# Optimization experiments

Hardware: AMD Instinct MI355X
Metric: run time of the kernel (lower is better)

The kernel has to match this reference:

```python
import jax, jax.numpy as jnp
import numpy as np

EOS = 1  # EOS_VALUE in the original code (word_label == 1 triggers end_sentence)
L_LAYERS = 2
B, T, H, E = 128, 256, 1024, 1024  # TD == E == input_size


def setup_inputs() -> dict:
    key = jax.random.key(0)
    ks = jax.random.split(key, 20)
    k = 1.0 / np.sqrt(H)
    u = lambda kk, shape: jax.random.uniform(kk, shape, jnp.float32, -k, k)
    inp = {
        "yy_pad": jax.random.randint(ks[0], (B, T), 0, E, dtype=jnp.int32),
        "h_t": jax.random.normal(ks[1], (L_LAYERS, B, H), jnp.float32),
        "h_t_rev": jax.random.normal(ks[2], (L_LAYERS, B, H), jnp.float32),
        "x_lens": jax.random.randint(ks[3], (B,), 1, T - 1, dtype=jnp.int32).at[0].set(T - 1),
        # parameters (layer 0 input size == E == H, so weights stack cleanly)
        "emb": jax.random.normal(ks[4], (E, E), jnp.float32) * 0.02,
        "W_ih": u(ks[5], (L_LAYERS, 4 * H, E)),
        "W_hh": u(ks[6], (L_LAYERS, 4 * H, H)),
        "b_ih": u(ks[7], (L_LAYERS, 4 * H)),
        "b_hh": u(ks[8], (L_LAYERS, 4 * H)),
        "W_ih_rev": u(ks[9], (L_LAYERS, 4 * H, E)),
        "W_hh_rev": u(ks[10], (L_LAYERS, 4 * H, H)),
        "b_ih_rev": u(ks[11], (L_LAYERS, 4 * H)),
        "b_hh_rev": u(ks[12], (L_LAYERS, 4 * H)),
        "c0": jnp.zeros((L_LAYERS, H), jnp.float32),
        "c0_rev": jnp.zeros((L_LAYERS, H), jnp.float32),
        "fc_W": u(ks[13], (E, 2 * H)),
        "fc_b": u(ks[14], (E,)),
    }
    return inp


def _lstm_cell(x, h, c, Wih, Whh, bih, bhh):
    # torch.nn.LSTMCell gate order: input, forget, cell(g), output
    z = x @ Wih.T + bih + h @ Whh.T + bhh  # [B, 4H]
    i, f, g, o = jnp.split(z, 4, axis=-1)
    c2 = jax.nn.sigmoid(f) * c + jax.nn.sigmoid(i) * jnp.tanh(g)
    h2 = jax.nn.sigmoid(o) * jnp.tanh(c2)
    return h2, c2


def reference(yy_pad, h_t, h_t_rev, x_lens, emb, W_ih, W_hh, b_ih, b_hh,
              W_ih_rev, W_hh_rev, b_ih_rev, b_hh_rev, c0, c0_rev, fc_W, fc_b):
    batch = yy_pad.shape[0]
    n_steps = yy_pad.shape[1]  # == max(x_lens) + 1 by construction (static)
    eos_onehot = jax.nn.one_hot(EOS, fc_W.shape[0], dtype=fc_W.dtype)  # [TD]

    c_init = jnp.broadcast_to(c0[:, None, :], (L_LAYERS, batch, c0.shape[1]))
    c_init_rev = jnp.broadcast_to(c0_rev[:, None, :], (L_LAYERS, batch, c0.shape[1]))

    def step(carry, _):
        feed, h, hr, c, cr, ended = carry
        x = emb[feed]   # [B, E]  (sos embedding / previous argmax token)
        xr = x
        hs, hrs, cs, crs = [], [], [], []
        for l in range(L_LAYERS):
            hn, cn = _lstm_cell(x, h[l], c[l], W_ih[l], W_hh[l], b_ih[l], b_hh[l])
            hrn, crn = _lstm_cell(xr, hr[l], cr[l], W_ih_rev[l], W_hh_rev[l], b_ih_rev[l], b_hh_rev[l])
            hs.append(hn); cs.append(cn); hrs.append(hrn); crs.append(crn)
            x, xr = hn, hrn
        h, hr = jnp.stack(hs), jnp.stack(hrs)
        c, cr = jnp.stack(cs), jnp.stack(crs)
        # faithful to torch: cat([B,H],[B,H]) -> [B,2H] -> permute(1,0) -> reshape(B,-1)
        wh = jnp.concatenate([h[-1], hr[-1]], axis=-1).T.reshape(batch, -1)
        logits = wh @ fc_W.T + fc_b  # [B, TD]
        logits = jnp.where(ended[:, None], eos_onehot, logits)
        label = jnp.argmax(logits, axis=1).astype(jnp.int32)
        ended = ended | (label == EOS)
        return (label, h, hr, c, cr, ended), logits

    carry0 = (yy_pad[:, 0], h_t, h_t_rev, c_init, c_init_rev,
              jnp.zeros((batch,), jnp.bool_))
    _, logits_seq = jax.lax.scan(step, carry0, None, length=n_steps)  # [T, B, TD]
    return jax.nn.softmax(jnp.transpose(logits_seq, (1, 0, 2)), axis=-1)  # [B, T, TD]
```

## Files before the change

### kernel.cpp

```cpp
#include <hip/hip_runtime.h>
#include <math.h>

#define NB 128
#define NT 256
#define NH 1024
#define NE 1024
#define G4 4096
#define EOSL 1

#define C_OFF    ((size_t)0)
#define HT_OFF   ((size_t)524288)
#define FCZ_OFF  ((size_t)786432)
#define BIAS_OFF ((size_t)2883584)
#define END_OFF  ((size_t)2899968)
#define XPH_OFF  ((size_t)2900096)
#define XPX_OFF  ((size_t)3948672)
#define WP_OFF   ((size_t)4079744)
#define TOTAL_MIN_F  ((size_t)4079744)
#define TOTAL_PACK_F ((size_t)37634176)

typedef __attribute__((ext_vector_type(8))) short s8v;
typedef __attribute__((ext_vector_type(4))) float f4v;

__device__ __forceinline__ float sigmoid_stable(float x) {
  if (x >= 0.f) return 1.f / (1.f + expf(-x));
  float ex = expf(x);
  return ex / (1.f + ex);
}
__device__ __forceinline__ void add4(float4& d, const float4 a) {
  d.x += a.x; d.y += a.y; d.z += a.z; d.w += a.w;
}
__device__ __forceinline__ unsigned short bf_rne(float x) {
  unsigned u = __float_as_uint(x);
  return (unsigned short)((u + 0x7FFFu + ((u >> 16) & 1u)) >> 16);
}
__device__ __forceinline__ void split_bf(float x, unsigned short& h, unsigned short& l) {
  unsigned u = __float_as_uint(x);
  unsigned hb = (u + 0x7FFFu + ((u >> 16) & 1u)) >> 16;
  h = (unsigned short)hb;
  float r = x - __uint_as_float(hb << 16);
  l = bf_rne(r);
}
__device__ __forceinline__ void cvt8(float4 a0, float4 a1, s8v& hi, s8v& lo)
{
  const float v[8] = {a0.x, a0.y, a0.z, a0.w, a1.x, a1.y, a1.z, a1.w};
  #pragma unroll
  for (int j = 0; j < 8; j++) {
    unsigned short h, l; split_bf(v[j], h, l);
    hi[j] = (short)h; lo[j] = (short)l;
  }
}


__global__ void k_init(const int* yy, const float* h_t, const float* h_tr,
                       const float* c0, const float* c0r,
                       const float* b_ih, const float* b_hh,
                       const float* b_ihr, const float* b_hhr,
                       const float* emb,
                       unsigned short* xph, unsigned short* xpx,
                       float* call, float* bias, int* ended)
{
  int idx = blockIdx.x * 256 + threadIdx.x;
  if (idx < 2 * 2048 * 128) {
    int dir = idx / (2048 * 128); int rem = idx % (2048 * 128);
    int row = rem >> 7, b = rem & 127;
    int l = row >> 10, n = row & 1023;
    const float* src = dir ? h_tr : h_t;
    float v = src[((size_t)l * 128 + b) * 1024 + n];
    unsigned short h, lo; split_bf(v, h, lo);
    size_t off = ((size_t)(dir * 64 + (row >> 5)) * 8 + (b >> 4)) * 1024
               + ((b & 15) + 16 * ((n >> 3) & 3)) * 8 + (n & 7);
    xph[off] = h; xph[off + 512] = lo;
  }
  if (idx < 4 * 1024 * 128) {
    int ld = idx / (1024 * 128); int l = ld >> 1;
    int rem = idx % (1024 * 128);
    int n = rem >> 7;
    const float* cs = (ld & 1) ? c0r : c0;
    call[idx] = cs[l * 1024 + n];
  }
  if (idx < 4 * 4096) {
    int ld = idx / 4096; int l = ld >> 1, dir = ld & 1;
    int m = idx & 4095;
    bias[idx] = (dir ? b_ihr : b_ih)[l * 4096 + m] + (dir ? b_hhr : b_hh)[l * 4096 + m];
  }
  if (idx < 128 * 1024) {
    int b = idx >> 10, k = idx & 1023;
    int e = yy[b * NT];
    float v = emb[(size_t)e * 1024 + k];
    unsigned short h, lo; split_bf(v, h, lo);
    size_t off = ((size_t)(k >> 5) * 8 + (b >> 4)) * 1024
               + ((b & 15) + 16 * ((k >> 3) & 3)) * 8 + (k & 7);
    xpx[off] = h; xpx[off + 512] = lo;
  }
  if (idx < NB) ended[idx] = 0;
}

__global__ void k_packW(const float* W_ih, const float* W_hh,
                        const float* W_ihr, const float* W_hhr,
                        unsigned short* WP)
{
  int idx = blockIdx.x * 256 + threadIdx.x;
  int l = idx & 63;
  int frag = idx >> 6;
  int ktile = frag & 63;
  int mq = (frag >> 6) & 255;
  int ld = frag >> 14;
  int layer = ld >> 1, dir = ld & 1;
  int s = l & 15;
  int gate = s >> 2;
  int m = gate * 1024 + mq * 4 + (s & 3);
  int kg = ktile * 32 + (l >> 4) * 8;
  const float* base;
  if (kg < 1024) base = (dir ? W_ihr : W_ih) + ((size_t)layer * 4096 + m) * 1024 + kg;
  else           base = (dir ? W_hhr : W_hh) + ((size_t)layer * 4096 + m) * 1024 + (kg - 1024);
  float4 a0 = *(const float4*)base, a1 = *(const float4*)(base + 4);
  s8v hi, lo; cvt8(a0, a1, hi, lo);
  unsigned short* outp = WP + (size_t)frag * 1024 + l * 8;
  *(s8v*)outp = hi;
  *(s8v*)(outp + 512) = lo;
}

__device__ __forceinline__ void red_write8(float* red, int slot, int l, const f4v (&acc)[8])
{
  #pragma unroll
  for (int bt = 0; bt < 8; bt++)
    *(f4v*)&red[(size_t)slot * 2048 + bt * 256 + l * 4] = acc[bt];
}
__device__ __forceinline__ void red_add8(const float* red, int slot, int l, f4v (&acc)[8])
{
  #pragma unroll
  for (int bt = 0; bt < 8; bt++)
    acc[bt] += *(const f4v*)&red[(size_t)slot * 2048 + bt * 256 + l * 4];
}
__device__ __forceinline__ void gloadB(const unsigned short* Bb, int kk,
                                       s8v (&h)[8], s8v (&lo)[8])
{
  #pragma unroll
  for (int bt = 0; bt < 8; bt++) {
    const unsigned short* q = Bb + ((size_t)(kk * 8 + bt) << 10);
    h[bt] = *(const s8v*)q; lo[bt] = *(const s8v*)(q + 512);
  }
}

struct CellP {
  const unsigned short* WP;
  const float* Wih; const float* Whh; const float* Wihr; const float* Whhr;
  const float* bias; float* c; const unsigned short* xpx; float* Ht;
};

template<int LAYER, int PACKED>
__global__ __launch_bounds__(512, 4) void k_cell(CellP p, const unsigned short* xpR,
                                                 unsigned short* xpW)
{
  __shared__ __align__(16) float lds[10240];
  const int mq = blockIdx.x, dir = blockIdx.y, tid = threadIdx.x;
  const int l = tid & 63, w = tid >> 6;
  const int lr = l & 15, lk = l >> 4;

  const unsigned short* Bb;
  if (LAYER == 0)
    Bb = (w < 4) ? p.xpx + (size_t)w * 65536
                 : xpR + (size_t)(dir * 64 + (w - 4) * 8) * 8192;
  else
    Bb = (w < 4) ? xpW + (size_t)(dir * 64 + w * 8) * 8192
                 : xpR + (size_t)(dir * 64 + 32 + (w - 4) * 8) * 8192;
  Bb += l * 8;

  f4v acc[8];
  #pragma unroll
  for (int bt = 0; bt < 8; bt++) acc[bt] = (f4v)(0.0f);

  if (PACKED) {
    const unsigned short* Wb = p.WP + (size_t)(LAYER * 2 + dir) * 16777216ULL
        + (((size_t)mq * 64 + (size_t)w * 8) << 10) + l * 8;
    s8v whc = *(const s8v*)Wb, wlc = *(const s8v*)(Wb + 512);
    #pragma unroll 1
    for (int kk = 0; kk < 8; kk++) {
      s8v bh[8], bl[8];
      gloadB(Bb, kk, bh, bl);
      s8v whn, wln;
      if (kk < 7) {
        const unsigned short* q = Wb + ((size_t)(kk + 1) << 10);
        whn = *(const s8v*)q; wln = *(const s8v*)(q + 512);
      }
      #pragma unroll
      for (int bt = 0; bt < 8; bt++) {
        acc[bt] = __builtin_amdgcn_mfma_f32_16x16x32_bf16(whc, bh[bt], acc[bt], 0, 0, 0);
        acc[bt] = __builtin_amdgcn_mfma_f32_16x16x32_bf16(whc, bl[bt], acc[bt], 0, 0, 0);
        acc[bt] = __builtin_amdgcn_mfma_f32_16x16x32_bf16(wlc, bh[bt], acc[bt], 0, 0, 0);
      }
      if (kk < 7) { whc = whn; wlc = wln; }
    }
  } else {
    const float* Wsel = ((w < 4) ? (dir ? p.Wihr : p.Wih) : (dir ? p.Whhr : p.Whh))
                      + (size_t)LAYER * 4194304;
    int col0 = (w & 3) * 256 + lk * 8;
    int m = (lr >> 2) * 1024 + mq * 4 + (lr & 3);
    const float* Wr = Wsel + (size_t)m * 1024 + col0;
    float4 ac0 = *(const float4*)Wr, ac1 = *(const float4*)(Wr + 4);
    #pragma unroll 1
    for (int kk = 0; kk < 8; kk++) {
      s8v bh[8], bl[8];
      gloadB(Bb, kk, bh, bl);
      float4 an0, an1;
      if (kk < 7) {
        an0 = *(const float4*)(Wr + (kk + 1) * 32);
        an1 = *(const float4*)(Wr + (kk + 1) * 32 + 4);
      }
      s8v wh, wl;
      cvt8(ac0, ac1, wh, wl);
      #pragma unroll
      for (int bt = 0; bt < 8; bt++) {
        acc[bt] = __builtin_amdgcn_mfma_f32_16x16x32_bf16(wh, bh[bt], acc[bt], 0, 0, 0);
        acc[bt] = __builtin_amdgcn_mfma_f32_16x16x32_bf16(wh, bl[bt], acc[bt], 0, 0, 0);
        acc[bt] = __builtin_amdgcn_mfma_f32_16x16x32_bf16(wl, bh[bt], acc[bt], 0, 0, 0);
      }
      if (kk < 7) { ac0 = an0; ac1 = an1; }
    }
  }

  if (w >= 4) red_write8(lds, w - 4, l, acc);
  __syncthreads();
  if (w < 4) red_add8(lds, w, l, acc);
  __syncthreads();
  if (w == 2 || w == 3) red_write8(lds, w - 2, l, acc);
  __syncthreads();
  if (w < 2) red_add8(lds, w, l, acc);
  __syncthreads();
  if (w < 2) red_write8(lds, w, l, acc);
  __syncthreads();
  float* zs = lds + 8192;
  {
    f4v s = *(const f4v*)&lds[(size_t)tid * 4];
    s += *(const f4v*)&lds[2048 + (size_t)tid * 4];
    int bt = tid >> 6, ll = tid & 63;
    #pragma unroll
    for (int r = 0; r < 4; r++)
      zs[((ll >> 4) * 4 + r) * 128 + bt * 16 + (ll & 15)] = s[r];
  }
  __syncthreads();

  {
    int ldg = LAYER * 2 + dir;
    int b = tid & 127, nl = tid >> 7;
    int n = mq * 4 + nl;
    float iv = zs[nl * 128 + b]        + p.bias[ldg * 4096 + n];
    float fv = zs[(4 + nl) * 128 + b]  + p.bias[ldg * 4096 + 1024 + n];
    float gv = zs[(8 + nl) * 128 + b]  + p.bias[ldg * 4096 + 2048 + n];
    float ov = zs[(12 + nl) * 128 + b] + p.bias[ldg * 4096 + 3072 + n];
    float* cp = p.c + ((size_t)ldg * 1024 + n) * 128 + b;
    float cold = *cp;
    float cn = sigmoid_stable(fv) * cold + sigmoid_stable(iv) * tanhf(gv);
    float hn = sigmoid_stable(ov) * tanhf(cn);
    *cp = cn;
    unsigned short hh, lo; split_bf(hn, hh, lo);
    int kt = LAYER * 32 + (n >> 5), n5 = n & 31;
    size_t off = ((size_t)(dir * 64 + kt) * 8 + (b >> 4)) * 1024
               + ((size_t)((b & 15) + 16 * ((n5 >> 3) & 3))) * 8 + (n5 & 7);
    xpW[off] = hh;
    xpW[off + 512] = lo;
    if (LAYER == 1)
      p.Ht[(size_t)dir * 131072 + (size_t)n * 128 + b] = hn;
  }
}

__global__ __launch_bounds__(256) void k_fc(const float* Ht, const float* fc_W, float* fcz)
{
  int et = blockIdx.x, kp = blockIdx.y;
  int e0 = et * 64;
  int k00 = kp * 128;
  __shared__ __align__(16) float in_s[128][36];
  __shared__ __align__(16) float w_s[64][36];
  int t = threadIdx.x, e_sub = t & 7, bg = t >> 3, b0 = bg * 4;
  float acc[8][4] = {};
  for (int kc = 0; kc < 128; kc += 32) {
    #pragma unroll
    for (int i = 0; i < 4; i++) {
      int flat = t + 256 * i, r = flat >> 3, f4i = flat & 7;
      float4 v = *(const float4*)(Ht + (size_t)r * 2048 + k00 + kc + f4i * 4);
      int sw = (f4i ^ (r >> 2)) & 7;
      *(float4*)&in_s[r][sw * 4] = v;
    }
    #pragma unroll
    for (int i = 0; i < 2; i++) {
      int flat = t + 256 * i, r = flat >> 3, f4i = flat & 7;
      *(float4*)&w_s[r][f4i * 4] =
          *(const float4*)(fc_W + (size_t)(e0 + r) * 2048 + k00 + kc + f4i * 4);
    }
    __syncthreads();
    #pragma unroll
    for (int kq = 0; kq < 8; kq++) {
      int ksw = (kq ^ bg) & 7;
      float4 a4[4];
      #pragma unroll
      for (int ib = 0; ib < 4; ib++) a4[ib] = *(const float4*)&in_s[b0 + ib][ksw * 4];
      float4 w4[8];
      #pragma unroll
      for (int je = 0; je < 8; je++) w4[je] = *(const float4*)&w_s[e_sub + 8 * je][kq * 4];
      #pragma unroll
      for (int je = 0; je < 8; je++)
        #pragma unroll
        for (int ib = 0; ib < 4; ib++)
          acc[je][ib] += a4[ib].x * w4[je].x + a4[ib].y * w4[je].y +
                         a4[ib].z * w4[je].z + a4[ib].w * w4[je].w;
    }
    __syncthreads();
  }
  for (int je = 0; je < 8; je++) {
    int e = e0 + e_sub + 8 * je;
    for (int ib = 0; ib < 4; ib++)
      fcz[((size_t)kp * NB + b0 + ib) * NE + e] = acc[je][ib];
  }
}

__global__ void k_final(const float* fcz, const float* fc_b, int* ended,
                        float* out, int tstep, const float* emb, unsigned short* xpx)
{
  int b = blockIdx.x;
  int t = threadIdx.x;
  __shared__ float sval[256];
  __shared__ int   sidx[256];
  __shared__ float ssum[256];
  bool end = (ended[b] != 0);
  float v[4];
  int e_base = t * 4;
  float4 vv = *(const float4*)&fc_b[e_base];
  #pragma unroll
  for (int p = 0; p < 16; p++)
    add4(vv, *(const float4*)&fcz[((size_t)p * NB + b) * NE + e_base]);
  v[0] = vv.x; v[1] = vv.y; v[2] = vv.z; v[3] = vv.w;
  if (end) {
    #pragma unroll
    for (int j = 0; j < 4; j++) v[j] = (e_base + j == EOSL) ? 1.f : 0.f;
  }
  float bv = v[0]; int bi = e_base;
  #pragma unroll
  for (int j = 1; j < 4; j++) if (v[j] > bv) { bv = v[j]; bi = e_base + j; }
  sval[t] = bv; sidx[t] = bi;
  __syncthreads();
  for (int s = 128; s > 0; s >>= 1) {
    if (t < s) {
      float ov = sval[t + s]; int oi = sidx[t + s];
      if (ov > sval[t] || (ov == sval[t] && oi < sidx[t])) { sval[t] = ov; sidx[t] = oi; }
    }
    __syncthreads();
  }
  float m = sval[0]; int label = sidx[0];
  {
    int k0 = t * 4;
    float4 e4 = *(const float4*)(emb + (size_t)label * 1024 + k0);
    size_t off = ((size_t)(k0 >> 5) * 8 + (b >> 4)) * 1024
               + ((b & 15) + 16 * ((k0 >> 3) & 3)) * 8 + (k0 & 7);
    ushort4 h4, l4;
    unsigned short hh, ll;
    split_bf(e4.x, hh, ll); h4.x = hh; l4.x = ll;
    split_bf(e4.y, hh, ll); h4.y = hh; l4.y = ll;
    split_bf(e4.z, hh, ll); h4.z = hh; l4.z = ll;
    split_bf(e4.w, hh, ll); h4.w = hh; l4.w = ll;
    *(ushort4*)(xpx + off) = h4;
    *(ushort4*)(xpx + off + 512) = l4;
  }
  float ls = 0.f;
  #pragma unroll
  for (int j = 0; j < 4; j++) { v[j] = expf(v[j] - m); ls += v[j]; }
  ssum[t] = ls;
  __syncthreads();
  for (int s = 128; s > 0; s >>= 1) { if (t < s) ssum[t] += ssum[t + s]; __syncthreads(); }
  float inv = 1.f / ssum[0];
  float* orow = out + ((size_t)b * NT + tstep) * NE + e_base;
  #pragma unroll
  for (int j = 0; j < 4; j++) orow[j] = v[j] * inv;
  if (t == 0) ended[b] = (end || label == EOSL) ? 1 : 0;
}

extern "C" void kernel_launch(void* const* d_in, const int* in_sizes, int n_in,
                              void* d_out, int out_size, void* d_ws, size_t ws_size,
                              hipStream_t stream)
{
  const int*   yy    = (const int*)d_in[0];
  const float* h_t   = (const float*)d_in[1];
  const float* h_tr  = (const float*)d_in[2];
  const float* emb   = (const float*)d_in[4];
  const float* W_ih  = (const float*)d_in[5];
  const float* W_hh  = (const float*)d_in[6];
  const float* b_ih  = (const float*)d_in[7];
  const float* b_hh  = (const float*)d_in[8];
  const float* W_ihr = (const float*)d_in[9];
  const float* W_hhr = (const float*)d_in[10];
  const float* b_ihr = (const float*)d_in[11];
  const float* b_hhr = (const float*)d_in[12];
  const float* c0    = (const float*)d_in[13];
  const float* c0r   = (const float*)d_in[14];
  const float* fc_W  = (const float*)d_in[15];
  const float* fc_b  = (const float*)d_in[16];
  float* out = (float*)d_out;

  float* ws = (float*)d_ws;
  float* call = ws + C_OFF;
  float* Ht   = ws + HT_OFF;
  float* fcz  = ws + FCZ_OFF;
  float* bias = ws + BIAS_OFF;
  int* ended  = (int*)(ws + END_OFF);
  unsigned short* xph = (unsigned short*)(ws + XPH_OFF);
  unsigned short* xpx = (unsigned short*)(ws + XPX_OFF);
  unsigned short* WP  = (unsigned short*)(ws + WP_OFF);
  bool packed = ws_size >= TOTAL_PACK_F * sizeof(float);

  k_init<<<2048, 256, 0, stream>>>(yy, h_t, h_tr, c0, c0r, b_ih, b_hh, b_ihr, b_hhr,
                                   emb, xph, xpx, call, bias, ended);
  if (packed)
    k_packW<<<16384, 256, 0, stream>>>(W_ih, W_hh, W_ihr, W_hhr, WP);

  CellP cp;
  cp.WP = WP;
  cp.Wih = W_ih; cp.Whh = W_hh; cp.Wihr = W_ihr; cp.Whhr = W_hhr;
  cp.bias = bias; cp.c = call; cp.xpx = xpx; cp.Ht = Ht;

  for (int t = 0; t < NT; t++) {
    const unsigned short* xpR = xph + (size_t)(t & 1) * 1048576;
    unsigned short* xpW = xph + (size_t)((t & 1) ^ 1) * 1048576;
    if (packed) {
      k_cell<0, 1><<<dim3(256, 2), 512, 0, stream>>>(cp, xpR, xpW);
      k_cell<1, 1><<<dim3(256, 2), 512, 0, stream>>>(cp, xpR, xpW);
    } else {
      k_cell<0, 0><<<dim3(256, 2), 512, 0, stream>>>(cp, xpR, xpW);
      k_cell<1, 0><<<dim3(256, 2), 512, 0, stream>>>(cp, xpR, xpW);
    }
    k_fc<<<dim3(16, 16), 256, 0, stream>>>(Ht, fc_W, fcz);
    k_final<<<128, 256, 0, stream>>>(fcz, fc_b, ended, out, t, emb, xpx);
  }
}
```

Measured before the change: 21.25 ms.

## Replace FP32 FC GEMM with split-bf16 MFMA kernel writing pre-packed fragments

```diff
diff --git a/kernel.cpp b/kernel.cpp
--- a/kernel.cpp
+++ b/kernel.cpp
@@ -9,15 +9,16 @@
 #define EOSL 1
 
 #define C_OFF    ((size_t)0)
-#define HT_OFF   ((size_t)524288)
-#define FCZ_OFF  ((size_t)786432)
-#define BIAS_OFF ((size_t)2883584)
-#define END_OFF  ((size_t)2899968)
-#define XPH_OFF  ((size_t)2900096)
-#define XPX_OFF  ((size_t)3948672)
-#define WP_OFF   ((size_t)4079744)
-#define TOTAL_MIN_F  ((size_t)4079744)
-#define TOTAL_PACK_F ((size_t)37634176)
+#define FCL_OFF  ((size_t)524288)
+#define XFC_OFF  ((size_t)655360)
+#define BIAS_OFF ((size_t)917504)
+#define END_OFF  ((size_t)933888)
+#define XPH_OFF  ((size_t)934016)
+#define XPX_OFF  ((size_t)1982592)
+#define FCWP_OFF ((size_t)2113664)
+#define WP_OFF   ((size_t)4210816)
+#define TOTAL_MIN_F  ((size_t)4210816)
+#define TOTAL_PACK_F ((size_t)37765248)
 
 typedef __attribute__((ext_vector_type(8))) short s8v;
 typedef __attribute__((ext_vector_type(4))) float f4v;
@@ -26,9 +27,6 @@
   if (x >= 0.f) return 1.f / (1.f + expf(-x));
   float ex = expf(x);
   return ex / (1.f + ex);
-}
-__device__ __forceinline__ void add4(float4& d, const float4 a) {
-  d.x += a.x; d.y += a.y; d.z += a.z; d.w += a.w;
 }
 __device__ __forceinline__ unsigned short bf_rne(float x) {
   unsigned u = __float_as_uint(x);
@@ -98,27 +96,43 @@
 
 __global__ void k_packW(const float* W_ih, const float* W_hh,
                         const float* W_ihr, const float* W_hhr,
-                        unsigned short* WP)
+                        const float* fc_W,
+                        unsigned short* WP, unsigned short* fcWP)
 {
   int idx = blockIdx.x * 256 + threadIdx.x;
-  int l = idx & 63;
-  int frag = idx >> 6;
-  int ktile = frag & 63;
-  int mq = (frag >> 6) & 255;
-  int ld = frag >> 14;
-  int layer = ld >> 1, dir = ld & 1;
-  int s = l & 15;
-  int gate = s >> 2;
-  int m = gate * 1024 + mq * 4 + (s & 3);
-  int kg = ktile * 32 + (l >> 4) * 8;
-  const float* base;
-  if (kg < 1024) base = (dir ? W_ihr : W_ih) + ((size_t)layer * 4096 + m) * 1024 + kg;
-  else           base = (dir ? W_hhr : W_hh) + ((size_t)layer * 4096 + m) * 1024 + (kg - 1024);
-  float4 a0 = *(const float4*)base, a1 = *(const float4*)(base + 4);
-  s8v hi, lo; cvt8(a0, a1, hi, lo);
-  unsigned short* outp = WP + (size_t)frag * 1024 + l * 8;
-  *(s8v*)outp = hi;
-  *(s8v*)(outp + 512) = lo;
+  if (idx < 4194304) {
+    int l = idx & 63;
+    int frag = idx >> 6;
+    int ktile = frag & 63;
+    int mq = (frag >> 6) & 255;
+    int ld = frag >> 14;
+    int layer = ld >> 1, dir = ld & 1;
+    int s = l & 15;
+    int gate = s >> 2;
+    int m = gate * 1024 + mq * 4 + (s & 3);
+    int kg = ktile * 32 + (l >> 4) * 8;
+    const float* base;
+    if (kg < 1024) base = (dir ? W_ihr : W_ih) + ((size_t)layer * 4096 + m) * 1024 + kg;
+    else           base = (dir ? W_hhr : W_hh) + ((size_t)layer * 4096 + m) * 1024 + (kg - 1024);
+    float4 a0 = *(const float4*)base, a1 = *(const float4*)(base + 4);
+    s8v hi, lo; cvt8(a0, a1, hi, lo);
+    unsigned short* outp = WP + (size_t)frag * 1024 + l * 8;
+    *(s8v*)outp = hi;
+    *(s8v*)(outp + 512) = lo;
+  } else if (idx < 4456448) {
+    int i2 = idx - 4194304;
+    int l = i2 & 63;
+    int frag = i2 >> 6;
+    int ktile = frag & 63, mq = frag >> 6;
+    int m = mq * 16 + (l & 15);
+    int kg = ktile * 32 + (l >> 4) * 8;
+    const float* base = fc_W + (size_t)m * 2048 + kg;
+    float4 a0 = *(const float4*)base, a1 = *(const float4*)(base + 4);
+    s8v hi, lo; cvt8(a0, a1, hi, lo);
+    unsigned short* outp = fcWP + (size_t)frag * 1024 + l * 8;
+    *(s8v*)outp = hi;
+    *(s8v*)(outp + 512) = lo;
+  }
 }
 
 __device__ __forceinline__ void red_write8(float* red, int slot, int l, const f4v (&acc)[8])
@@ -142,11 +156,35 @@
     h[bt] = *(const s8v*)q; lo[bt] = *(const s8v*)(q + 512);
   }
 }
+__device__ __forceinline__ void reduce8_to_zs(float* lds, int tid, int l, int w,
+                                              f4v (&acc)[8])
+{
+  if (w >= 4) red_write8(lds, w - 4, l, acc);
+  __syncthreads();
+  if (w < 4) red_add8(lds, w, l, acc);
+  __syncthreads();
+  if (w == 2 || w == 3) red_write8(lds, w - 2, l, acc);
+  __syncthreads();
+  if (w < 2) red_add8(lds, w, l, acc);
+  __syncthreads();
+  if (w < 2) red_write8(lds, w, l, acc);
+  __syncthreads();
+  float* zs = lds + 8192;
+  {
+    f4v s = *(const f4v*)&lds[(size_t)tid * 4];
+    s += *(const f4v*)&lds[2048 + (size_t)tid * 4];
+    int bt = tid >> 6, ll = tid & 63;
+    #pragma unroll
+    for (int r = 0; r < 4; r++)
+      zs[((ll >> 4) * 4 + r) * 128 + bt * 16 + (ll & 15)] = s[r];
+  }
+  __syncthreads();
+}
 
 struct CellP {
   const unsigned short* WP;
   const float* Wih; const float* Whh; const float* Wihr; const float* Whhr;
-  const float* bias; float* c; const unsigned short* xpx; float* Ht;
+  const float* bias; float* c; const unsigned short* xpx; unsigned short* xfc;
 };
 
 template<int LAYER, int PACKED>
@@ -220,26 +258,8 @@
     }
   }
 
-  if (w >= 4) red_write8(lds, w - 4, l, acc);
-  __syncthreads();
-  if (w < 4) red_add8(lds, w, l, acc);
-  __syncthreads();
-  if (w == 2 || w == 3) red_write8(lds, w - 2, l, acc);
-  __syncthreads();
-  if (w < 2) red_add8(lds, w, l, acc);
-  __syncthreads();
-  if (w < 2) red_write8(lds, w, l, acc);
-  __syncthreads();
+  reduce8_to_zs(lds, tid, l, w, acc);
   float* zs = lds + 8192;
-  {
-    f4v s = *(const f4v*)&lds[(size_t)tid * 4];
-    s += *(const f4v*)&lds[2048 + (size_t)tid * 4];
-    int bt = tid >> 6, ll = tid & 63;
-    #pragma unroll
-    for (int r = 0; r < 4; r++)
-      zs[((ll >> 4) * 4 + r) * 128 + bt * 16 + (ll & 15)] = s[r];
-  }
-  __syncthreads();
 
   {
     int ldg = LAYER * 2 + dir;
@@ -260,62 +280,92 @@
                + ((size_t)((b & 15) + 16 * ((n5 >> 3) & 3))) * 8 + (n5 & 7);
     xpW[off] = hh;
     xpW[off + 512] = lo;
-    if (LAYER == 1)
-      p.Ht[(size_t)dir * 131072 + (size_t)n * 128 + b] = hn;
-  }
-}
-
-__global__ __launch_bounds__(256) void k_fc(const float* Ht, const float* fc_W, float* fcz)
-{
-  int et = blockIdx.x, kp = blockIdx.y;
-  int e0 = et * 64;
-  int k00 = kp * 128;
-  __shared__ __align__(16) float in_s[128][36];
-  __shared__ __align__(16) float w_s[64][36];
-  int t = threadIdx.x, e_sub = t & 7, bg = t >> 3, b0 = bg * 4;
-  float acc[8][4] = {};
-  for (int kc = 0; kc < 128; kc += 32) {
+    if (LAYER == 1) {
+      int bo = dir * 64 + (n >> 4);
+      int k = (n & 15) * 128 + b;
+      size_t fo = ((size_t)((k >> 5) * 8 + (bo >> 4))) * 1024
+                + ((size_t)((bo & 15) + 16 * ((k >> 3) & 3))) * 8 + (k & 7);
+      p.xfc[fo] = hh;
+      p.xfc[fo + 512] = lo;
+    }
+  }
+}
+
+template<int PACKED>
+__global__ __launch_bounds__(512, 4) void k_fcm(const unsigned short* fcWP, const float* fcW,
+                                                const unsigned short* xfc, const float* fcb,
+                                                float* fcl)
+{
+  __shared__ __align__(16) float lds[10240];
+  const int mq = blockIdx.x, tid = threadIdx.x;
+  const int l = tid & 63, w = tid >> 6;
+  const int lr = l & 15, lk = l >> 4;
+  const unsigned short* Bb = xfc + (((size_t)w * 64) << 10) + l * 8;
+
+  f4v acc[8];
+  #pragma unroll
+  for (int bt = 0; bt < 8; bt++) acc[bt] = (f4v)(0.0f);
+
+  if (PACKED) {
+    const unsigned short* Wb = fcWP + (((size_t)mq * 64 + (size_t)w * 8) << 10) + l * 8;
+    s8v whc = *(const s8v*)Wb, wlc = *(const s8v*)(Wb + 512);
+    #pragma unroll 1
+    for (int kk = 0; kk < 8; kk++) {
+      s8v bh[8], bl[8];
+      gloadB(Bb, kk, bh, bl);
+      s8v whn, wln;
+      if (kk < 7) {
+        const unsigned short* q = Wb + ((size_t)(kk + 1) << 10);
+        whn = *(const s8v*)q; wln = *(const s8v*)(q + 512);
+      }
+      #pragma unroll
+      for (int bt = 0; bt < 8; bt++) {
+        acc[bt] = __builtin_amdgcn_mfma_f32_16x16x32_bf16(whc, bh[bt], acc[bt], 0, 0, 0);
+        acc[bt] = __builtin_amdgcn_mfma_f32_16x16x32_bf16(whc, bl[bt], acc[bt], 0, 0, 0);
+        acc[bt] = __builtin_amdgcn_mfma_f32_16x16x32_bf16(wlc, bh[bt], acc[bt], 0, 0, 0);
+      }
+      if (kk < 7) { whc = whn; wlc = wln; }
+    }
+  } else {
+    int m = mq * 16 + lr;
+    const float* Wr = fcW + (size_t)m * 2048 + w * 256 + lk * 8;
+    float4 ac0 = *(const float4*)Wr, ac1 = *(const float4*)(Wr + 4);
+    #pragma unroll 1
+    for (int kk = 0; kk < 8; kk++) {
+      s8v bh[8], bl[8];
+      gloadB(Bb, kk, bh, bl);
+      float4 an0, an1;
+      if (kk < 7) {
+        an0 = *(const float4*)(Wr + (kk + 1) * 32);
+        an1 = *(const float4*)(Wr + (kk + 1) * 32 + 4);
+      }
+      s8v wh, wl;
+      cvt8(ac0, ac1, wh, wl);
+      #pragma unroll
+      for (int bt = 0; bt < 8; bt++) {
+        acc[bt] = __builtin_amdgcn_mfma_f32_16x16x32_bf16(wh, bh[bt], acc[bt], 0, 0, 0);
+        acc[bt] = __builtin_amdgcn_mfma_f32_16x16x32_bf16(wh, bl[bt], acc[bt], 0, 0, 0);
+        acc[bt] = __builtin_amdgcn_mfma_f32_16x16x32_bf16(wl, bh[bt], acc[bt], 0, 0, 0);
+      }
+      if (kk < 7) { ac0 = an0; ac1 = an1; }
+    }
+  }
+
+  reduce8_to_zs(lds, tid, l, w, acc);
+  float* zs = lds + 8192;
+
+  {
+    int bo = tid & 127, sg = tid >> 7;
+    f4v o;
     #pragma unroll
-    for (int i = 0; i < 4; i++) {
-      int flat = t + 256 * i, r = flat >> 3, f4i = flat & 7;
-      float4 v = *(const float4*)(Ht + (size_t)r * 2048 + k00 + kc + f4i * 4);
-      int sw = (f4i ^ (r >> 2)) & 7;
-      *(float4*)&in_s[r][sw * 4] = v;
-    }
-    #pragma unroll
-    for (int i = 0; i < 2; i++) {
-      int flat = t + 256 * i, r = flat >> 3, f4i = flat & 7;
-      *(float4*)&w_s[r][f4i * 4] =
-          *(const float4*)(fc_W + (size_t)(e0 + r) * 2048 + k00 + kc + f4i * 4);
-    }
-    __syncthreads();
-    #pragma unroll
-    for (int kq = 0; kq < 8; kq++) {
-      int ksw = (kq ^ bg) & 7;
-      float4 a4[4];
-      #pragma unroll
-      for (int ib = 0; ib < 4; ib++) a4[ib] = *(const float4*)&in_s[b0 + ib][ksw * 4];
-      float4 w4[8];
-      #pragma unroll
-      for (int je = 0; je < 8; je++) w4[je] = *(const float4*)&w_s[e_sub + 8 * je][kq * 4];
-      #pragma unroll
-      for (int je = 0; je < 8; je++)
-        #pragma unroll
-        for (int ib = 0; ib < 4; ib++)
-          acc[je][ib] += a4[ib].x * w4[je].x + a4[ib].y * w4[je].y +
-                         a4[ib].z * w4[je].z + a4[ib].w * w4[je].w;
-    }
-    __syncthreads();
-  }
-  for (int je = 0; je < 8; je++) {
-    int e = e0 + e_sub + 8 * je;
-    for (int ib = 0; ib < 4; ib++)
-      fcz[((size_t)kp * NB + b0 + ib) * NE + e] = acc[je][ib];
-  }
-}
-
-__global__ void k_final(const float* fcz, const float* fc_b, int* ended,
-                        float* out, int tstep, const float* emb, unsigned short* xpx)
+    for (int r = 0; r < 4; r++)
+      o[r] = zs[(sg * 4 + r) * 128 + bo] + fcb[mq * 16 + sg * 4 + r];
+    *(f4v*)(fcl + (size_t)bo * 1024 + mq * 16 + sg * 4) = o;
+  }
+}
+
+__global__ void k_final(const float* fcl, int* ended, float* out, int tstep,
+                        const float* emb, unsigned short* xpx)
 {
   int b = blockIdx.x;
   int t = threadIdx.x;
@@ -325,10 +375,7 @@
   bool end = (ended[b] != 0);
   float v[4];
   int e_base = t * 4;
-  float4 vv = *(const float4*)&fc_b[e_base];
-  #pragma unroll
-  for (int p = 0; p < 16; p++)
-    add4(vv, *(const float4*)&fcz[((size_t)p * NB + b) * NE + e_base]);
+  float4 vv = *(const float4*)&fcl[(size_t)b * 1024 + e_base];
   v[0] = vv.x; v[1] = vv.y; v[2] = vv.z; v[3] = vv.w;
   if (end) {
     #pragma unroll
@@ -398,24 +445,25 @@
 
   float* ws = (float*)d_ws;
   float* call = ws + C_OFF;
-  float* Ht   = ws + HT_OFF;
-  float* fcz  = ws + FCZ_OFF;
+  float* fcl  = ws + FCL_OFF;
   float* bias = ws + BIAS_OFF;
   int* ended  = (int*)(ws + END_OFF);
-  unsigned short* xph = (unsigned short*)(ws + XPH_OFF);
-  unsigned short* xpx = (unsigned short*)(ws + XPX_OFF);
-  unsigned short* WP  = (unsigned short*)(ws + WP_OFF);
+  unsigned short* xfc  = (unsigned short*)(ws + XFC_OFF);
+  unsigned short* xph  = (unsigned short*)(ws + XPH_OFF);
+  unsigned short* xpx  = (unsigned short*)(ws + XPX_OFF);
+  unsigned short* fcWP = (unsigned short*)(ws + FCWP_OFF);
+  unsigned short* WP   = (unsigned short*)(ws + WP_OFF);
   bool packed = ws_size >= TOTAL_PACK_F * sizeof(float);
 
   k_init<<<2048, 256, 0, stream>>>(yy, h_t, h_tr, c0, c0r, b_ih, b_hh, b_ihr, b_hhr,
                                    emb, xph, xpx, call, bias, ended);
   if (packed)
-    k_packW<<<16384, 256, 0, stream>>>(W_ih, W_hh, W_ihr, W_hhr, WP);
+    k_packW<<<17408, 256, 0, stream>>>(W_ih, W_hh, W_ihr, W_hhr, fc_W, WP, fcWP);
 
   CellP cp;
   cp.WP = WP;
   cp.Wih = W_ih; cp.Whh = W_hh; cp.Wihr = W_ihr; cp.Whhr = W_hhr;
-  cp.bias = bias; cp.c = call; cp.xpx = xpx; cp.Ht = Ht;
+  cp.bias = bias; cp.c = call; cp.xpx = xpx; cp.xfc = xfc;
 
   for (int t = 0; t < NT; t++) {
     const unsigned short* xpR = xph + (size_t)(t & 1) * 1048576;
@@ -423,11 +471,12 @@
     if (packed) {
       k_cell<0, 1><<<dim3(256, 2), 512, 0, stream>>>(cp, xpR, xpW);
       k_cell<1, 1><<<dim3(256, 2), 512, 0, stream>>>(cp, xpR, xpW);
+      k_fcm<1><<<64, 512, 0, stream>>>(fcWP, fc_W, xfc, fc_b, fcl);
     } else {
       k_cell<0, 0><<<dim3(256, 2), 512, 0, stream>>>(cp, xpR, xpW);
       k_cell<1, 0><<<dim3(256, 2), 512, 0, stream>>>(cp, xpR, xpW);
-    }
-    k_fc<<<dim3(16, 16), 256, 0, stream>>>(Ht, fc_W, fcz);
-    k_final<<<128, 256, 0, stream>>>(fcz, fc_b, ended, out, t, emb, xpx);
-  }
-}
+      k_fcm<0><<<64, 512, 0, stream>>>(fcWP, fc_W, xfc, fc_b, fcl);
+    }
+    k_final<<<128, 256, 0, stream>>>(fcl, ended, out, t, emb, xpx);
+  }
+}
```

After: 19.26 ms. 1.1x faster.
